# Performance work log

Hardware: AMD Instinct MI355X
Metric: run time of the kernel (lower is better)

Reference implementation:

```python
import jax, jax.numpy as jnp
import numpy as np

N_POINTS = 1_000_000
N_SEG = 50_000


def setup_inputs() -> dict:
    key = jax.random.key(0)
    ks = jax.random.split(key, 8)

    def w(k, shape):
        fan_in = shape[0]
        return jax.random.normal(k, shape, dtype=jnp.float32) * (1.0 / np.sqrt(fan_in))

    return {
        "x": jax.random.normal(ks[0], (N_POINTS, 11), dtype=jnp.float32),
        "idx": jax.random.randint(ks[1], (N_POINTS,), 0, N_SEG, dtype=jnp.int32),
        "W0": w(ks[2], (11, 64)),   "b0": jnp.zeros((64,), jnp.float32),
        "W1": w(ks[3], (64, 128)),  "b1": jnp.zeros((128,), jnp.float32),
        "W2": w(ks[4], (128, 256)), "b2": jnp.zeros((256,), jnp.float32),
        "W3": w(ks[5], (256, 256)), "b3": jnp.zeros((256,), jnp.float32),
        "W4": w(ks[6], (256, 128)), "b4": jnp.zeros((128,), jnp.float32),
        "Wh": w(ks[7], (128, 13)),  "bh": jnp.zeros((13,), jnp.float32),
    }


def _mlp_layer(x, W, b):
    # PointMLP layer: Linear -> activation (BN folded into linear at inference)
    return jax.nn.relu(x @ W + b)


def reference(x, idx, W0, b0, W1, b1, W2, b2, W3, b3, W4, b4, Wh, bh):
    # local_nn: pointwise MLP on every point
    h = _mlp_layer(x, W0, b0)          # [N, 64]
    h = _mlp_layer(h, W1, b1)          # [N, 128]
    h = _mlp_layer(h, W2, b2)          # [N, 256]
    # scatter(x, idx, dim=0, reduce='max') -> segment max pooling
    g = jax.ops.segment_max(h, idx, num_segments=N_SEG)  # [S, 256]
    g = jnp.where(jnp.isfinite(g), g, 0.0)  # empty segments -> 0
    # global_nn on pooled segment features
    g = _mlp_layer(g, W3, b3)          # [S, 256]
    g = _mlp_layer(g, W4, b4)          # [S, 128]
    # classifier head (logits)
    return g @ Wh + bh                 # [S, 13]
```

## Files before the change

### kernel.cpp

```cpp
#include <hip/hip_runtime.h>
#include <hip/hip_bf16.h>

#define NPTS 1000000
#define NSEG 50000
#define SPB  8
#define LDP  36

typedef __attribute__((ext_vector_type(8))) short bf16x8;
typedef __attribute__((ext_vector_type(4))) float f32x4;

union F4 { float4 v; float f[4]; };

__device__ __forceinline__ unsigned short f2bf(float f) {
    union { __hip_bfloat16 h; unsigned short u; } cv;
    cv.h = __float2bfloat16(f);
    return cv.u;
}
__device__ __forceinline__ float bf2f(unsigned short u) {
    union { unsigned short u; __hip_bfloat16 h; } cv;
    cv.u = u;
    return __bfloat162float(cv.h);
}

#define MFMA16(a, b, c) __builtin_amdgcn_mfma_f32_16x16x32_bf16(a, b, c, 0, 0, 0)

__global__ __launch_bounds__(256) void hist_kernel(const int* __restrict__ idx,
                                                   unsigned* __restrict__ counts) {
    int i = blockIdx.x * blockDim.x + threadIdx.x;
    for (; i < NPTS; i += gridDim.x * blockDim.x) atomicAdd(&counts[idx[i]], 1u);
}

__global__ __launch_bounds__(1024) void scan1_kernel(const unsigned* __restrict__ counts,
                                                     unsigned* __restrict__ start,
                                                     unsigned* __restrict__ bsum) {
    __shared__ unsigned tmp[1024];
    const int t = threadIdx.x;
    const int i = blockIdx.x * 1024 + t;
    unsigned v = (i < NSEG) ? counts[i] : 0u;
    tmp[t] = v;
    __syncthreads();
    for (int off = 1; off < 1024; off <<= 1) {
        unsigned add = (t >= off) ? tmp[t - off] : 0u;
        __syncthreads();
        tmp[t] += add;
        __syncthreads();
    }
    if (i < NSEG) start[i] = tmp[t] - v;
    if (t == 1023) bsum[blockIdx.x] = tmp[1023];
}

__global__ __launch_bounds__(64) void scan2_kernel(unsigned* __restrict__ bsum,
                                                   unsigned* __restrict__ boff,
                                                   int nblk) {
    const int t = threadIdx.x;
    unsigned v = (t < nblk) ? bsum[t] : 0u;
    unsigned own = v;
    for (int off = 1; off < 64; off <<= 1) {
        unsigned u = __shfl_up(v, off, 64);
        if (t >= off) v += u;
    }
    if (t < nblk) boff[t] = v - own;
}

__global__ __launch_bounds__(1024) void scan3_kernel(unsigned* __restrict__ start,
                                                     const unsigned* __restrict__ boff) {
    const int i = blockIdx.x * 1024 + threadIdx.x;
    if (i < NSEG) start[i] += boff[blockIdx.x];
}

__global__ __launch_bounds__(256) void scatter_kernel(const int* __restrict__ idx,
                                                      unsigned* __restrict__ start,
                                                      unsigned* __restrict__ perm) {
    int i = blockIdx.x * blockDim.x + threadIdx.x;
    for (; i < NPTS; i += gridDim.x * blockDim.x) {
        int s = idx[i];
        unsigned pos = atomicAdd(&start[s], 1u);
        perm[pos] = (unsigned)i;
    }
}

__global__ __launch_bounds__(256) void pack_weights(const float* __restrict__ W1,
                                                    const float* __restrict__ W2,
                                                    const float* __restrict__ Wh,
                                                    const float* __restrict__ W3,
                                                    const float* __restrict__ W4,
                                                    unsigned short* __restrict__ wp,
                                                    unsigned short* __restrict__ wp34,
                                                    int total) {
    int i = blockIdx.x * 256 + threadIdx.x;
    for (; i < total; i += gridDim.x * 256) {
        if (i < 43008) {
            if (i < 8192) {
                int e = i & 7, l = (i >> 3) & 63, kt = (i >> 9) & 1, nt = i >> 10;
                int k = kt * 32 + (l >> 4) * 8 + e, n = nt * 16 + (l & 15);
                wp[i] = f2bf(W1[k * 128 + n]);
            } else if (i < 40960) {
                int j = i - 8192;
                int e = j & 7, l = (j >> 3) & 63, kt = (j >> 9) & 3, nt = j >> 11;
                int k = kt * 32 + (l >> 4) * 8 + e, n = nt * 16 + (l & 15);
                wp[i] = f2bf(W2[k * 256 + n]);
            } else {
                int j = i - 40960;
                int e = j & 7, l = (j >> 3) & 63, kt = j >> 9;
                int k = kt * 32 + (l >> 4) * 8 + e, n = l & 15;
                wp[i] = (n < 13) ? f2bf(Wh[k * 13 + n]) : 0;
            }
        } else {
            int i2 = i - 43008;
            if (i2 < 65536) {
                int e = i2 & 7, l = (i2 >> 3) & 63, kt = (i2 >> 9) & 7, nt = i2 >> 12;
                int k = kt * 32 + (l >> 4) * 8 + e, n = nt * 16 + (l & 15);
                wp34[i2] = f2bf(W3[k * 256 + n]);
            } else {
                int j = i2 - 65536;
                int e = j & 7, l = (j >> 3) & 63, kt = (j >> 9) & 7, nt = j >> 12;
                int k = kt * 32 + (l >> 4) * 8 + e, n = nt * 16 + (l & 15);
                wp34[i2] = f2bf(W4[k * 128 + n]);
            }
        }
    }
}

__global__ __launch_bounds__(256) void phase1m(
    const float* __restrict__ x, const int* __restrict__ idx,
    const unsigned* __restrict__ endofs, const unsigned* __restrict__ perm,
    const float* __restrict__ W0, const float* __restrict__ b0,
    const unsigned short* __restrict__ wp,
    const float* __restrict__ b1, const float* __restrict__ b2,
    float* __restrict__ g)
{
    __shared__ __align__(16) unsigned short h1hi[32 * 72];
    __shared__ __align__(16) unsigned short h1lo[32 * 72];
    __shared__ __align__(16) unsigned short h2hi[32 * 136];
    __shared__ __align__(16) unsigned short h2lo[32 * 136];
    __shared__ float xsT[11][LDP];
    __shared__ float w0s[11 * 64];
    __shared__ unsigned gmax[SPB][264];
    __shared__ int segl[32];

    const int t    = threadIdx.x;
    const int lane = t & 63;
    const int w    = t >> 6;
    const int col  = lane & 15;
    const int grp  = lane >> 4;
    const int s0   = blockIdx.x * SPB;

    const unsigned A = (s0 == 0) ? 0u : endofs[s0 - 1];
    const unsigned B = endofs[s0 + SPB - 1];

    const int nt2 = w * 2;
    const int nt4 = w * 4;

    bf16x8 w1f[2][2], w2f[4][4];
    #pragma unroll
    for (int n = 0; n < 2; ++n)
        #pragma unroll
        for (int kt = 0; kt < 2; ++kt)
            w1f[n][kt] = *(const bf16x8*)&wp[(((nt2 + n) * 2 + kt) * 64 + lane) * 8];
    #pragma unroll
    for (int n = 0; n < 4; ++n)
        #pragma unroll
        for (int kt = 0; kt < 4; ++kt)
            w2f[n][kt] = *(const bf16x8*)&wp[8192 + (((nt4 + n) * 4 + kt) * 64 + lane) * 8];
    float bias1[2], bias2[4];
    #pragma unroll
    for (int n = 0; n < 2; ++n) bias1[n] = b1[(nt2 + n) * 16 + col];
    #pragma unroll
    for (int n = 0; n < 4; ++n) bias2[n] = b2[(nt4 + n) * 16 + col];

    const int p0 = (t & 7) << 2;
    const int j0 = (t >> 3) << 1;
    float bias0a = b0[j0], bias0b = b0[j0 + 1];

    for (int i = t; i < SPB * 264; i += 256) ((unsigned*)gmax)[i] = 0u;
    for (int i = t; i < 11 * 64; i += 256) w0s[i] = W0[i];
    __syncthreads();

    const int nchunk = (int)(B - A + 31u) >> 5;
    for (int c = 0; c < nchunk; ++c) {
        if (t < 32) {
            unsigned gp = A + ((unsigned)c << 5) + (unsigned)t;
            segl[t] = (gp < B) ? (idx[perm[gp]] - s0) : -1;
        }
        for (int i = t; i < 32 * 11; i += 256) {
            int p = i / 11, ch = i - p * 11;
            unsigned gp = A + ((unsigned)c << 5) + (unsigned)p;
            float v = 0.f;
            if (gp < B) v = x[perm[gp] * 11 + ch];
            xsT[ch][p] = v;
        }
        __syncthreads();

        {
            float acc0[2][4];
            #pragma unroll
            for (int pp = 0; pp < 4; ++pp) { acc0[0][pp] = bias0a; acc0[1][pp] = bias0b; }
            #pragma unroll
            for (int k = 0; k < 11; ++k) {
                F4 a; a.v = *(const float4*)&xsT[k][p0];
                float wv0 = w0s[k * 64 + j0];
                float wv1 = w0s[k * 64 + j0 + 1];
                #pragma unroll
                for (int pp = 0; pp < 4; ++pp) {
                    acc0[0][pp] = fmaf(a.f[pp], wv0, acc0[0][pp]);
                    acc0[1][pp] = fmaf(a.f[pp], wv1, acc0[1][pp]);
                }
            }
            #pragma unroll
            for (int pp = 0; pp < 4; ++pp) {
                int pt = p0 + pp;
                float v0 = fmaxf(acc0[0][pp], 0.f);
                float v1 = fmaxf(acc0[1][pp], 0.f);
                unsigned short h0 = f2bf(v0), h1v = f2bf(v1);
                unsigned short l0 = f2bf(v0 - bf2f(h0)), l1v = f2bf(v1 - bf2f(h1v));
                *(unsigned*)&h1hi[pt * 72 + j0] = (unsigned)h0 | ((unsigned)h1v << 16);
                *(unsigned*)&h1lo[pt * 72 + j0] = (unsigned)l0 | ((unsigned)l1v << 16);
            }
        }
        __syncthreads();

        {
            f32x4 acc[2][2];
            #pragma unroll
            for (int m = 0; m < 2; ++m)
                #pragma unroll
                for (int n = 0; n < 2; ++n) {
                    float b = bias1[n];
                    acc[m][n] = (f32x4){b, b, b, b};
                }
            #pragma unroll
            for (int kt = 0; kt < 2; ++kt) {
                bf16x8 ahi[2], alo[2];
                #pragma unroll
                for (int m = 0; m < 2; ++m) {
                    int off = (m * 16 + col) * 72 + kt * 32 + grp * 8;
                    ahi[m] = *(const bf16x8*)&h1hi[off];
                    alo[m] = *(const bf16x8*)&h1lo[off];
                }
                #pragma unroll
                for (int n = 0; n < 2; ++n)
                    #pragma unroll
                    for (int m = 0; m < 2; ++m) {
                        acc[m][n] = MFMA16(ahi[m], w1f[n][kt], acc[m][n]);
                        acc[m][n] = MFMA16(alo[m], w1f[n][kt], acc[m][n]);
                    }
            }
            #pragma unroll
            for (int m = 0; m < 2; ++m)
                #pragma unroll
                for (int n = 0; n < 2; ++n) {
                    int ch = (nt2 + n) * 16 + col;
                    #pragma unroll
                    for (int r = 0; r < 4; ++r) {
                        int pt = m * 16 + grp * 4 + r;
                        float v = fmaxf(acc[m][n][r], 0.f);
                        unsigned short hi = f2bf(v);
                        h2hi[pt * 136 + ch] = hi;
                        h2lo[pt * 136 + ch] = f2bf(v - bf2f(hi));
                    }
                }
        }
        __syncthreads();

        {
            f32x4 acc2[2][4];
            #pragma unroll
            for (int m = 0; m < 2; ++m)
                #pragma unroll
                for (int n = 0; n < 4; ++n) {
                    float b = bias2[n];
                    acc2[m][n] = (f32x4){b, b, b, b};
                }
            #pragma unroll
            for (int kt = 0; kt < 4; ++kt) {
                bf16x8 ahi[2], alo[2];
                #pragma unroll
                for (int m = 0; m < 2; ++m) {
                    int off = (m * 16 + col) * 136 + kt * 32 + grp * 8;
                    ahi[m] = *(const bf16x8*)&h2hi[off];
                    alo[m] = *(const bf16x8*)&h2lo[off];
                }
                #pragma unroll
                for (int n = 0; n < 4; ++n)
                    #pragma unroll
                    for (int m = 0; m < 2; ++m) {
                        acc2[m][n] = MFMA16(ahi[m], w2f[n][kt], acc2[m][n]);
                        acc2[m][n] = MFMA16(alo[m], w2f[n][kt], acc2[m][n]);
                    }
            }
            int slv[2][4];
            #pragma unroll
            for (int m = 0; m < 2; ++m)
                #pragma unroll
                for (int r = 0; r < 4; ++r)
                    slv[m][r] = segl[m * 16 + grp * 4 + r];
            #pragma unroll
            for (int m = 0; m < 2; ++m) {
                if (slv[m][0] < 0) continue;
                #pragma unroll
                for (int n = 0; n < 4; ++n) {
                    int ch = (nt4 + n) * 16 + col;
                    float v0 = fmaxf(acc2[m][n][0], 0.f);
                    float v1 = fmaxf(acc2[m][n][1], 0.f);
                    float v2 = fmaxf(acc2[m][n][2], 0.f);
                    float v3 = fmaxf(acc2[m][n][3], 0.f);
                    if (slv[m][0] == slv[m][3]) {
                        float mx = fmaxf(fmaxf(v0, v1), fmaxf(v2, v3));
                        atomicMax(&gmax[slv[m][0]][ch], __float_as_uint(mx));
                    } else {
                        atomicMax(&gmax[slv[m][0]][ch], __float_as_uint(v0));
                        if (slv[m][1] >= 0) atomicMax(&gmax[slv[m][1]][ch], __float_as_uint(v1));
                        if (slv[m][2] >= 0) atomicMax(&gmax[slv[m][2]][ch], __float_as_uint(v2));
                        if (slv[m][3] >= 0) atomicMax(&gmax[slv[m][3]][ch], __float_as_uint(v3));
                    }
                }
            }
        }
        __syncthreads();
    }

    for (int i = t; i < SPB * 256; i += 256) {
        int sl = i >> 8, ch = i & 255;
        g[(s0 + sl) * 256 + ch] = __uint_as_float(gmax[sl][ch]);
    }
}

__global__ __launch_bounds__(256) void phase2m(
    const float* __restrict__ g,
    const unsigned short* __restrict__ wp,
    const unsigned short* __restrict__ wp34,
    const float* __restrict__ b3, const float* __restrict__ b4,
    const float* __restrict__ bh,
    float* __restrict__ out)
{
    __shared__ __align__(16) unsigned short gThi[16 * 264];
    __shared__ __align__(16) unsigned short gTlo[16 * 264];
    __shared__ __align__(16) unsigned short h4hi[16 * 264];
    __shared__ __align__(16) unsigned short h4lo[16 * 264];
    __shared__ __align__(16) unsigned short h5hi[16 * 136];
    __shared__ __align__(16) unsigned short h5lo[16 * 136];

    const int t    = threadIdx.x;
    const int lane = t & 63;
    const int w    = t >> 6;
    const int col  = lane & 15;
    const int grp  = lane >> 4;
    const int seg0 = blockIdx.x * 16;

    for (int i = t; i < 16 * 64; i += 256) {
        int s = i >> 6, c4 = (i & 63) << 2;
        F4 v; v.v = *(const float4*)&g[(seg0 + s) * 256 + c4];
        unsigned short h[4], l[4];
        #pragma unroll
        for (int e = 0; e < 4; ++e) {
            h[e] = f2bf(v.f[e]);
            l[e] = f2bf(v.f[e] - bf2f(h[e]));
        }
        *(unsigned*)&gThi[s * 264 + c4]     = (unsigned)h[0] | ((unsigned)h[1] << 16);
        *(unsigned*)&gThi[s * 264 + c4 + 2] = (unsigned)h[2] | ((unsigned)h[3] << 16);
        *(unsigned*)&gTlo[s * 264 + c4]     = (unsigned)l[0] | ((unsigned)l[1] << 16);
        *(unsigned*)&gTlo[s * 264 + c4 + 2] = (unsigned)l[2] | ((unsigned)l[3] << 16);
    }
    __syncthreads();

    {
        f32x4 acc[4];
        #pragma unroll
        for (int n = 0; n < 4; ++n) {
            float b = b3[(w * 4 + n) * 16 + col];
            acc[n] = (f32x4){b, b, b, b};
        }
        #pragma unroll
        for (int kt = 0; kt < 8; ++kt) {
            int aoff = col * 264 + kt * 32 + grp * 8;
            bf16x8 ahi = *(const bf16x8*)&gThi[aoff];
            bf16x8 alo = *(const bf16x8*)&gTlo[aoff];
            #pragma unroll
            for (int n = 0; n < 4; ++n) {
                bf16x8 bw = *(const bf16x8*)&wp34[(((w * 4 + n) * 8 + kt) * 64 + lane) * 8];
                acc[n] = MFMA16(ahi, bw, acc[n]);
                acc[n] = MFMA16(alo, bw, acc[n]);
            }
        }
        #pragma unroll
        for (int n = 0; n < 4; ++n) {
            int ch = (w * 4 + n) * 16 + col;
            #pragma unroll
            for (int r = 0; r < 4; ++r) {
                int pt = grp * 4 + r;
                float v = fmaxf(acc[n][r], 0.f);
                unsigned short hi = f2bf(v);
                h4hi[pt * 264 + ch] = hi;
                h4lo[pt * 264 + ch] = f2bf(v - bf2f(hi));
            }
        }
    }
    __syncthreads();

    {
        f32x4 acc[2];
        #pragma unroll
        for (int n = 0; n < 2; ++n) {
            float b = b4[(w * 2 + n) * 16 + col];
            acc[n] = (f32x4){b, b, b, b};
        }
        #pragma unroll
        for (int kt = 0; kt < 8; ++kt) {
            int aoff = col * 264 + kt * 32 + grp * 8;
            bf16x8 ahi = *(const bf16x8*)&h4hi[aoff];
            bf16x8 alo = *(const bf16x8*)&h4lo[aoff];
            #pragma unroll
            for (int n = 0; n < 2; ++n) {
                bf16x8 bw = *(const bf16x8*)&wp34[65536 + (((w * 2 + n) * 8 + kt) * 64 + lane) * 8];
                acc[n] = MFMA16(ahi, bw, acc[n]);
                acc[n] = MFMA16(alo, bw, acc[n]);
            }
        }
        #pragma unroll
        for (int n = 0; n < 2; ++n) {
            int ch = (w * 2 + n) * 16 + col;
            #pragma unroll
            for (int r = 0; r < 4; ++r) {
                int pt = grp * 4 + r;
                float v = fmaxf(acc[n][r], 0.f);
                unsigned short hi = f2bf(v);
                h5hi[pt * 136 + ch] = hi;
                h5lo[pt * 136 + ch] = f2bf(v - bf2f(hi));
            }
        }
    }
    __syncthreads();

    if (w == 0) {
        float b = (col < 13) ? bh[col] : 0.f;
        f32x4 acc = (f32x4){b, b, b, b};
        #pragma unroll
        for (int kt = 0; kt < 4; ++kt) {
            int aoff = col * 136 + kt * 32 + grp * 8;
            bf16x8 ahi = *(const bf16x8*)&h5hi[aoff];
            bf16x8 alo = *(const bf16x8*)&h5lo[aoff];
            bf16x8 bw = *(const bf16x8*)&wp[40960 + ((kt * 64 + lane) * 8)];
            acc = MFMA16(ahi, bw, acc);
            acc = MFMA16(alo, bw, acc);
        }
        if (col < 13) {
            #pragma unroll
            for (int r = 0; r < 4; ++r)
                out[(seg0 + grp * 4 + r) * 13 + col] = acc[r];
        }
    }
}

__global__ __launch_bounds__(256) void phase2(
    const float* __restrict__ g,
    const float* __restrict__ W3, const float* __restrict__ b3,
    const float* __restrict__ W4, const float* __restrict__ b4,
    const float* __restrict__ Wh, const float* __restrict__ bh,
    float* __restrict__ out)
{
    __shared__ float gT[256][LDP];
    __shared__ float h4T[256][LDP];

    const int t = threadIdx.x;
    const long base = (long)blockIdx.x * 32;

    for (int i = t; i < 32 * 256; i += 256) {
        int s = i >> 8, c = i & 255;
        float v = 0.f;
        if (base + s < NSEG) v = g[(base + s) * 256 + c];
        gT[c][s] = v;
    }
    __syncthreads();

    const int p0 = (t & 7) << 2;
    const int jg = t >> 3;

    {
        const int j0 = jg << 3;
        float acc[8][4];
        #pragma unroll
        for (int jj = 0; jj < 8; ++jj) {
            float b = b3[j0 + jj];
            #pragma unroll
            for (int pp = 0; pp < 4; ++pp) acc[jj][pp] = b;
        }
        #pragma unroll 4
        for (int k = 0; k < 256; ++k) {
            F4 a;  a.v  = *(const float4*)&gT[k][p0];
            F4 wa; wa.v = *(const float4*)&W3[k * 256 + j0];
            F4 wb; wb.v = *(const float4*)&W3[k * 256 + j0 + 4];
            #pragma unroll
            for (int jj = 0; jj < 4; ++jj)
                #pragma unroll
                for (int pp = 0; pp < 4; ++pp) {
                    acc[jj][pp]     = fmaf(a.f[pp], wa.f[jj], acc[jj][pp]);
                    acc[jj + 4][pp] = fmaf(a.f[pp], wb.f[jj], acc[jj + 4][pp]);
                }
        }
        __syncthreads();
        #pragma unroll
        for (int jj = 0; jj < 8; ++jj) {
            F4 v;
            #pragma unroll
            for (int pp = 0; pp < 4; ++pp) v.f[pp] = fmaxf(acc[jj][pp], 0.f);
            *(float4*)&h4T[j0 + jj][p0] = v.v;
        }
    }
    __syncthreads();

    float (*h5T)[LDP] = gT;
    {
        const int j0 = jg << 2;
        float acc[4][4];
        #pragma unroll
        for (int jj = 0; jj < 4; ++jj) {
            float b = b4[j0 + jj];
            #pragma unroll
            for (int pp = 0; pp < 4; ++pp) acc[jj][pp] = b;
        }
        #pragma unroll 4
        for (int k = 0; k < 256; ++k) {
            F4 a; a.v = *(const float4*)&h4T[k][p0];
            F4 w; w.v = *(const float4*)&W4[k * 128 + j0];
            #pragma unroll
            for (int jj = 0; jj < 4; ++jj)
                #pragma unroll
                for (int pp = 0; pp < 4; ++pp)
                    acc[jj][pp] = fmaf(a.f[pp], w.f[jj], acc[jj][pp]);
        }
        #pragma unroll
        for (int jj = 0; jj < 4; ++jj) {
            F4 v;
            #pragma unroll
            for (int pp = 0; pp < 4; ++pp) v.f[pp] = fmaxf(acc[jj][pp], 0.f);
            *(float4*)&h5T[j0 + jj][p0] = v.v;
        }
    }
    __syncthreads();

    {
        #pragma unroll
        for (int pass = 0; pass < 2; ++pass) {
            int p = (t >> 4) + pass * 16;
            int j = t & 15;
            if (j < 13 && base + p < NSEG) {
                float acc = bh[j];
                #pragma unroll 4
                for (int k = 0; k < 128; ++k)
                    acc = fmaf(h5T[k][p], Wh[k * 13 + j], acc);
                out[(base + p) * 13 + j] = acc;
            }
        }
    }
}

extern "C" void kernel_launch(void* const* d_in, const int* in_sizes, int n_in,
                              void* d_out, int out_size, void* d_ws, size_t ws_size,
                              hipStream_t stream)
{
    const float* x  = (const float*)d_in[0];
    const int*   idx= (const int*)  d_in[1];
    const float* W0 = (const float*)d_in[2];
    const float* b0 = (const float*)d_in[3];
    const float* W1 = (const float*)d_in[4];
    const float* b1 = (const float*)d_in[5];
    const float* W2 = (const float*)d_in[6];
    const float* b2 = (const float*)d_in[7];
    const float* W3 = (const float*)d_in[8];
    const float* b3 = (const float*)d_in[9];
    const float* W4 = (const float*)d_in[10];
    const float* b4 = (const float*)d_in[11];
    const float* Wh = (const float*)d_in[12];
    const float* bh = (const float*)d_in[13];
    float* out = (float*)d_out;

    unsigned* counts = (unsigned*)d_ws;
    unsigned* start  = counts + 50048;
    unsigned* perm   = start + 50048;
    float*    g      = (float*)(perm + 1000000);
    unsigned short* wp   = (unsigned short*)counts;
    unsigned short* wp34 = (unsigned short*)(g + (size_t)NSEG * 256);
    unsigned* bsum = (unsigned*)g;
    unsigned* boff = bsum + 64;

    const size_t need34 = ((size_t)(perm + 1000000) - (size_t)d_ws)
                        + (size_t)NSEG * 256 * 4 + 98304 * 2;
    const bool useMfmaP2 = (ws_size >= need34);
    const int nblk = (NSEG + 1023) / 1024;

    hipMemsetAsync(counts, 0, NSEG * sizeof(unsigned), stream);
    hist_kernel <<<1024, 256, 0, stream>>>(idx, counts);
    scan1_kernel<<<nblk, 1024, 0, stream>>>(counts, start, bsum);
    scan2_kernel<<<1, 64, 0, stream>>>(bsum, boff, nblk);
    scan3_kernel<<<nblk, 1024, 0, stream>>>(start, boff);
    pack_weights<<<160, 256, 0, stream>>>(W1, W2, Wh, W3, W4, wp, wp34,
                                          useMfmaP2 ? 141312 : 43008);
    scatter_kernel<<<1024, 256, 0, stream>>>(idx, start, perm);
    phase1m<<<NSEG / SPB, 256, 0, stream>>>(x, idx, start, perm,
                                            W0, b0, wp, b1, b2, g);
    if (useMfmaP2) {
        phase2m<<<NSEG / 16, 256, 0, stream>>>(g, wp, wp34, b3, b4, bh, out);
    } else {
        phase2<<<(NSEG + 31) / 32, 256, 0, stream>>>(g, W3, b3, W4, b4, Wh, bh, out);
    }
}
```

Measured before the change: 610.6 us.

## Scatter input points into segment-sorted padded buffer and prefetch in phase1

The scatter pass now copies each point's 11 features into a segment-sorted buffer padded to 12 floats, so phase1 reads contiguous float4 rows instead of gathering through perm and x. The next chunk is prefetched into registers while the current one is computed, and each point's local segment id now comes from comparing its position against the segment boundaries rather than reloading idx through perm. In exchange the scatter kernel writes about 48 MB of scattered data and the workspace must be larger, with the old perm path kept as a fallback.

```diff
diff --git a/kernel.cpp b/kernel.cpp
--- a/kernel.cpp
+++ b/kernel.cpp
@@ -66,6 +66,21 @@
                                                      const unsigned* __restrict__ boff) {
     const int i = blockIdx.x * 1024 + threadIdx.x;
     if (i < NSEG) start[i] += boff[blockIdx.x];
+}
+
+__global__ __launch_bounds__(256) void scatter_x(const float* __restrict__ x,
+                                                 const int* __restrict__ idx,
+                                                 unsigned* __restrict__ start,
+                                                 float* __restrict__ xs12) {
+    int i = blockIdx.x * blockDim.x + threadIdx.x;
+    for (; i < NPTS; i += gridDim.x * blockDim.x) {
+        int s = idx[i];
+        unsigned pos = atomicAdd(&start[s], 1u);
+        const float* src = x + (size_t)i * 11;
+        float* dst = xs12 + (size_t)pos * 12;
+        #pragma unroll
+        for (int c = 0; c < 11; ++c) dst[c] = src[c];
+    }
 }
 
 __global__ __launch_bounds__(256) void scatter_kernel(const int* __restrict__ idx,
@@ -121,9 +136,10 @@
     }
 }
 
-__global__ __launch_bounds__(256) void phase1m(
-    const float* __restrict__ x, const int* __restrict__ idx,
-    const unsigned* __restrict__ endofs, const unsigned* __restrict__ perm,
+template<bool SX>
+__global__ __launch_bounds__(256) void phase1m2(
+    const float* __restrict__ xsrc, const unsigned* __restrict__ perm,
+    const unsigned* __restrict__ endofs,
     const float* __restrict__ W0, const float* __restrict__ b0,
     const unsigned short* __restrict__ wp,
     const float* __restrict__ b1, const float* __restrict__ b2,
@@ -133,7 +149,7 @@
     __shared__ __align__(16) unsigned short h1lo[32 * 72];
     __shared__ __align__(16) unsigned short h2hi[32 * 136];
     __shared__ __align__(16) unsigned short h2lo[32 * 136];
-    __shared__ float xsT[11][LDP];
+    __shared__ float xsT[12][LDP];
     __shared__ float w0s[11 * 64];
     __shared__ unsigned gmax[SPB][264];
     __shared__ int segl[32];
@@ -146,7 +162,10 @@
     const int s0   = blockIdx.x * SPB;
 
     const unsigned A = (s0 == 0) ? 0u : endofs[s0 - 1];
-    const unsigned B = endofs[s0 + SPB - 1];
+    unsigned bnd[SPB];
+    #pragma unroll
+    for (int s = 0; s < SPB; ++s) bnd[s] = endofs[s0 + s];
+    const unsigned B = bnd[SPB - 1];
 
     const int nt2 = w * 2;
     const int nt4 = w * 4;
@@ -177,19 +196,43 @@
     __syncthreads();
 
     const int nchunk = (int)(B - A + 31u) >> 5;
+
+    const float4* xs4 = (const float4*)xsrc;
+    float4 xreg = make_float4(0.f, 0.f, 0.f, 0.f);
+    if (SX && nchunk > 0 && t < 96) xreg = xs4[(size_t)A * 3 + t];
+
     for (int c = 0; c < nchunk; ++c) {
+        if constexpr (SX) {
+            if (t < 96) {
+                int p = t / 3, j = t - p * 3;
+                xsT[4 * j + 0][p] = xreg.x;
+                xsT[4 * j + 1][p] = xreg.y;
+                xsT[4 * j + 2][p] = xreg.z;
+                xsT[4 * j + 3][p] = xreg.w;
+            }
+        } else {
+            for (int i = t; i < 32 * 11; i += 256) {
+                int p = i / 11, ch = i - p * 11;
+                unsigned gp = A + ((unsigned)c << 5) + (unsigned)p;
+                float v = 0.f;
+                if (gp < B) v = xsrc[(size_t)perm[gp] * 11 + ch];
+                xsT[ch][p] = v;
+            }
+        }
         if (t < 32) {
             unsigned gp = A + ((unsigned)c << 5) + (unsigned)t;
-            segl[t] = (gp < B) ? (idx[perm[gp]] - s0) : -1;
-        }
-        for (int i = t; i < 32 * 11; i += 256) {
-            int p = i / 11, ch = i - p * 11;
-            unsigned gp = A + ((unsigned)c << 5) + (unsigned)p;
-            float v = 0.f;
-            if (gp < B) v = x[perm[gp] * 11 + ch];
-            xsT[ch][p] = v;
+            int sl = -1;
+            if (gp < B) {
+                sl = 0;
+                #pragma unroll
+                for (int s = 0; s < SPB - 1; ++s) sl += (gp >= bnd[s]) ? 1 : 0;
+            }
+            segl[t] = sl;
         }
         __syncthreads();
+
+        if (SX && (c + 1 < nchunk) && t < 96)
+            xreg = xs4[((size_t)A + ((size_t)(c + 1) << 5)) * 3 + t];
 
         {
             float acc0[2][4];
@@ -321,7 +364,7 @@
 
     for (int i = t; i < SPB * 256; i += 256) {
         int sl = i >> 8, ch = i & 255;
-        g[(s0 + sl) * 256 + ch] = __uint_as_float(gmax[sl][ch]);
+        g[(size_t)(s0 + sl) * 256 + ch] = __uint_as_float(gmax[sl][ch]);
     }
 }
 
@@ -349,7 +392,7 @@
 
     for (int i = t; i < 16 * 64; i += 256) {
         int s = i >> 6, c4 = (i & 63) << 2;
-        F4 v; v.v = *(const float4*)&g[(seg0 + s) * 256 + c4];
+        F4 v; v.v = *(const float4*)&g[(size_t)(seg0 + s) * 256 + c4];
         unsigned short h[4], l[4];
         #pragma unroll
         for (int e = 0; e < 4; ++e) {
@@ -446,7 +489,7 @@
         if (col < 13) {
             #pragma unroll
             for (int r = 0; r < 4; ++r)
-                out[(seg0 + grp * 4 + r) * 13 + col] = acc[r];
+                out[(size_t)(seg0 + grp * 4 + r) * 13 + col] = acc[r];
         }
     }
 }
@@ -576,31 +619,52 @@
 
     unsigned* counts = (unsigned*)d_ws;
     unsigned* start  = counts + 50048;
-    unsigned* perm   = start + 50048;
-    float*    g      = (float*)(perm + 1000000);
-    unsigned short* wp   = (unsigned short*)counts;
-    unsigned short* wp34 = (unsigned short*)(g + (size_t)NSEG * 256);
-    unsigned* bsum = (unsigned*)g;
-    unsigned* boff = bsum + 64;
-
-    const size_t need34 = ((size_t)(perm + 1000000) - (size_t)d_ws)
-                        + (size_t)NSEG * 256 * 4 + 98304 * 2;
-    const bool useMfmaP2 = (ws_size >= need34);
+    unsigned short* wp = (unsigned short*)counts;
+
+    const size_t need_x = (50048ull + 50048 + 12000000 + 12800000) * 4 + 98304 * 2;
+    const size_t need_p = (50048ull + 50048 + 1000000 + 12800000) * 4 + 98304 * 2;
+
+    const bool fitX = (ws_size >= need_x);
     const int nblk = (NSEG + 1023) / 1024;
 
     hipMemsetAsync(counts, 0, NSEG * sizeof(unsigned), stream);
     hist_kernel <<<1024, 256, 0, stream>>>(idx, counts);
-    scan1_kernel<<<nblk, 1024, 0, stream>>>(counts, start, bsum);
-    scan2_kernel<<<1, 64, 0, stream>>>(bsum, boff, nblk);
-    scan3_kernel<<<nblk, 1024, 0, stream>>>(start, boff);
-    pack_weights<<<160, 256, 0, stream>>>(W1, W2, Wh, W3, W4, wp, wp34,
-                                          useMfmaP2 ? 141312 : 43008);
-    scatter_kernel<<<1024, 256, 0, stream>>>(idx, start, perm);
-    phase1m<<<NSEG / SPB, 256, 0, stream>>>(x, idx, start, perm,
-                                            W0, b0, wp, b1, b2, g);
-    if (useMfmaP2) {
+
+    if (fitX) {
+        float*    xs12 = (float*)(start + 50048);
+        float*    g    = xs12 + 12000000;
+        unsigned short* wp34 = (unsigned short*)(g + (size_t)NSEG * 256);
+        unsigned* bsum = (unsigned*)g;
+        unsigned* boff = bsum + 64;
+
+        scan1_kernel<<<nblk, 1024, 0, stream>>>(counts, start, bsum);
+        scan2_kernel<<<1, 64, 0, stream>>>(bsum, boff, nblk);
+        scan3_kernel<<<nblk, 1024, 0, stream>>>(start, boff);
+        pack_weights<<<160, 256, 0, stream>>>(W1, W2, Wh, W3, W4, wp, wp34, 141312);
+        scatter_x   <<<3907, 256, 0, stream>>>(x, idx, start, xs12);
+        phase1m2<true><<<NSEG / SPB, 256, 0, stream>>>(xs12, nullptr, start,
+                                                       W0, b0, wp, b1, b2, g);
         phase2m<<<NSEG / 16, 256, 0, stream>>>(g, wp, wp34, b3, b4, bh, out);
     } else {
-        phase2<<<(NSEG + 31) / 32, 256, 0, stream>>>(g, W3, b3, W4, b4, Wh, bh, out);
-    }
-}
+        unsigned* perm = start + 50048;
+        float*    g    = (float*)(perm + 1000000);
+        unsigned short* wp34 = (unsigned short*)(g + (size_t)NSEG * 256);
+        unsigned* bsum = (unsigned*)g;
+        unsigned* boff = bsum + 64;
+        const bool useMfmaP2 = (ws_size >= need_p);
+
+        scan1_kernel<<<nblk, 1024, 0, stream>>>(counts, start, bsum);
+        scan2_kernel<<<1, 64, 0, stream>>>(bsum, boff, nblk);
+        scan3_kernel<<<nblk, 1024, 0, stream>>>(start, boff);
+        pack_weights<<<160, 256, 0, stream>>>(W1, W2, Wh, W3, W4, wp, wp34,
+                                              useMfmaP2 ? 141312 : 43008);
+        scatter_kernel<<<1024, 256, 0, stream>>>(idx, start, perm);
+        phase1m2<false><<<NSEG / SPB, 256, 0, stream>>>(x, perm, start,
+                                                        W0, b0, wp, b1, b2, g);
+        if (useMfmaP2) {
+            phase2m<<<NSEG / 16, 256, 0, stream>>>(g, wp, wp34, b3, b4, bh, out);
+        } else {
+            phase2<<<(NSEG + 31) / 32, 256, 0, stream>>>(g, W3, b3, W4, b4, Wh, bh, out);
+        }
+    }
+}
```

Result: faster. 508.8 us (-16.7%).
